# Optimization experiments

Measured on AMD Instinct MI355X. Metric: run time of the kernel, lower is better.

The kernel has to match this reference:

```python
import jax, jax.numpy as jnp
import numpy as np

B, C, W, H = 8, 64, 256, 256


def setup_inputs() -> dict:
    key = jax.random.key(0)
    ks = jax.random.split(key, 7)
    s = lambda n: 1.0 / np.sqrt(n)
    return {
        "x": jax.random.normal(ks[0], (B, C, W, H), dtype=jnp.float32),
        "Wc": jax.random.uniform(ks[1], (C, C), jnp.float32, -s(C), s(C)),
        "bc": jax.random.uniform(ks[2], (C,), jnp.float32, -s(C), s(C)),
        "Ww": jax.random.uniform(ks[3], (W, W), jnp.float32, -s(W), s(W)),
        "bw": jax.random.uniform(ks[4], (W,), jnp.float32, -s(W), s(W)),
        "Wh": jax.random.uniform(ks[5], (H, H), jnp.float32, -s(H), s(H)),
        "bh": jax.random.uniform(ks[6], (H,), jnp.float32, -s(H), s(H)),
    }


def reference(x, Wc, bc, Ww, bw, Wh, bh):
    # SE-style gates: global avg-pool over the two non-gated dims, 1x1 conv
    # (= dense on pooled vector), sigmoid. x is (B, C, W, H).
    c = jax.nn.sigmoid(jnp.einsum("oc,bc->bo", Wc, x.mean((2, 3))) + bc)  # (B, C)
    w = jax.nn.sigmoid(jnp.einsum("ow,bw->bo", Ww, x.mean((1, 3))) + bw)  # (B, W)
    h = jax.nn.sigmoid(jnp.einsum("oh,bh->bo", Wh, x.mean((1, 2))) + bh)  # (B, H)
    # Rank-1 tensor (triple outer product) per batch, broadcast-fused:
    return c[:, :, None, None] * w[:, None, :, None] * h[:, None, None, :]
```

## Files before the change

### kernel.cpp

```cpp
#include <hip/hip_runtime.h>


#define NB 8
#define NC 64
#define NW 256
#define NH 256

typedef float f4v __attribute__((ext_vector_type(4)));


__global__ __launch_bounds__(256) void pool_kernel(const float* __restrict__ x,
                                                   float* __restrict__ ws) {
    float* sum_c = ws;
    float* sum_w = ws + 512;
    float* sum_h = ws + 2560;

    int k    = blockIdx.x;
    int bc   = k >> 2;
    int q    = k & 3;
    int b    = bc >> 6;
    int tid  = threadIdx.x;
    int wv   = tid >> 6;
    int lane = tid & 63;

    const f4v* xr = (const f4v*)x + (size_t)bc * (NW * (NH / 4))
                    + (size_t)(q * 64 + wv * 16) * (NH / 4) + lane;

    __shared__ float rowsum[4][16];
    __shared__ float cols[4][NH];
    __shared__ float wpart[4];

    f4v v[16];
    #pragma unroll
    for (int r = 0; r < 16; ++r) v[r] = xr[(size_t)r * (NH / 4)];

    f4v col = {0.f, 0.f, 0.f, 0.f};
    float rs[16];
    #pragma unroll
    for (int r = 0; r < 16; ++r) {
        col += v[r];
        rs[r] = (v[r][0] + v[r][1]) + (v[r][2] + v[r][3]);
    }
    #pragma unroll
    for (int off = 32; off; off >>= 1) {
        #pragma unroll
        for (int r = 0; r < 16; ++r) rs[r] += __shfl_xor(rs[r], off);
    }
    #pragma unroll
    for (int r = 0; r < 16; ++r)
        if (lane == r) rowsum[wv][r] = rs[r];

    cols[wv][lane * 4 + 0] = col[0];
    cols[wv][lane * 4 + 1] = col[1];
    cols[wv][lane * 4 + 2] = col[2];
    cols[wv][lane * 4 + 3] = col[3];
    __syncthreads();

    float cv = cols[0][tid] + cols[1][tid] + cols[2][tid] + cols[3][tid];
    atomicAdd(&sum_h[b * NH + tid], cv);

    if (tid < 64)
        atomicAdd(&sum_w[b * NW + q * 64 + tid], rowsum[tid >> 4][tid & 15]);

    float t = cv;
    #pragma unroll
    for (int off = 32; off; off >>= 1) t += __shfl_xor(t, off);
    if (lane == 0) wpart[wv] = t;
    __syncthreads();
    if (tid == 0) atomicAdd(&sum_c[bc], wpart[0] + wpart[1] + wpart[2] + wpart[3]);
}

__global__ __launch_bounds__(256) void gates_kernel(const float* __restrict__ Wc, const float* __restrict__ bc_,
                                                    const float* __restrict__ Ww, const float* __restrict__ bw_,
                                                    const float* __restrict__ Wh, const float* __restrict__ bh_,
                                                    float* __restrict__ ws) {
    const float* sum_c = ws;
    const float* sum_w = ws + 512;
    const float* sum_h = ws + 2560;
    float* gate_c = ws + 4608;
    float* gate_w = ws + 5120;
    float* gate_h = ws + 7168;

    int j = blockIdx.x * 4 + (threadIdx.x >> 6);
    int lane = threadIdx.x & 63;

    float acc = 0.f, bias;
    float* dst;
    if (j < 512) {
        int b = j >> 6, o = j & 63;
        acc = Wc[o * 64 + lane] * sum_c[b * 64 + lane] * (1.f / 65536.f);
        bias = bc_[o];
        dst = &gate_c[j];
    } else if (j < 2560) {
        int j2 = j - 512;
        int b = j2 >> 8, o = j2 & 255;
        const float* wr = Ww + o * 256;
        const float* sr = sum_w + b * 256;
        #pragma unroll
        for (int m = 0; m < 4; ++m) acc += wr[lane + 64 * m] * sr[lane + 64 * m];
        acc *= (1.f / 16384.f);
        bias = bw_[o];
        dst = &gate_w[j2];
    } else {
        int j2 = j - 2560;
        int b = j2 >> 8, o = j2 & 255;
        const float* wr = Wh + o * 256;
        const float* sr = sum_h + b * 256;
        #pragma unroll
        for (int m = 0; m < 4; ++m) acc += wr[lane + 64 * m] * sr[lane + 64 * m];
        acc *= (1.f / 16384.f);
        bias = bh_[o];
        dst = &gate_h[j2];
    }
    #pragma unroll
    for (int off = 32; off; off >>= 1) acc += __shfl_xor(acc, off);
    if (lane == 0) *dst = 1.f / (1.f + expf(-(acc + bias)));
}

__global__ __launch_bounds__(256) void out_kernel(const float* __restrict__ ws,
                                                  float* __restrict__ out) {
    const float* gate_c = ws + 4608;
    const float* gate_w = ws + 5120;
    const float4* gate_h4 = (const float4*)(ws + 7168);

    const size_t N4 = (size_t)NB * NC * NW * (NH / 4);
    size_t stride = (size_t)gridDim.x * blockDim.x;
    for (size_t i = (size_t)blockIdx.x * blockDim.x + threadIdx.x; i < N4; i += stride) {
        int h4 = (int)(i & 63);
        size_t row = i >> 6;
        int w = (int)(row & 255);
        size_t bcr = row >> 8;
        int c = (int)(bcr & 63);
        int b = (int)(bcr >> 6);
        float g = gate_c[b * 64 + c] * gate_w[b * 256 + w];
        float4 gh = gate_h4[b * 64 + h4];
        f4v val = {g * gh.x, g * gh.y, g * gh.z, g * gh.w};
        __builtin_nontemporal_store(val, (f4v*)(out + 4 * i));
    }
}

extern "C" void kernel_launch(void* const* d_in, const int* in_sizes, int n_in,
                              void* d_out, int out_size, void* d_ws, size_t ws_size,
                              hipStream_t stream) {
    const float* x   = (const float*)d_in[0];
    const float* Wc  = (const float*)d_in[1];
    const float* bc_ = (const float*)d_in[2];
    const float* Ww  = (const float*)d_in[3];
    const float* bw_ = (const float*)d_in[4];
    const float* Wh  = (const float*)d_in[5];
    const float* bh_ = (const float*)d_in[6];
    float* ws = (float*)d_ws;

    hipMemsetAsync(ws, 0, 4608 * sizeof(float), stream);

    pool_kernel<<<2048, 256, 0, stream>>>(x, ws);
    gates_kernel<<<4608 / 4, 256, 0, stream>>>(Wc, bc_, Ww, bw_, Wh, bh_, ws);
    out_kernel<<<2048, 256, 0, stream>>>(ws, (float*)d_out);
}
```

Measured before the change: 62.80 us.

## Restructure pool kernel into 512-thread blocks covering half a plane with interleaved rows

The pooling kernel now uses 1024 blocks of 512 threads, each reducing half of a (b,c) plane (128 rows), instead of 2048 blocks of 256 threads over a quarter plane. Rows are interleaved across the 8 waves and loaded in two batches of 8 using nontemporal loads, which cuts register pressure and halves the number of atomics on sum_h. The trade is fewer blocks in flight, less memory-level parallelism per thread, and a more complex shared-memory reduction.

```diff
diff --git a/kernel.cpp b/kernel.cpp
--- a/kernel.cpp
+++ b/kernel.cpp
@@ -9,46 +9,49 @@
 typedef float f4v __attribute__((ext_vector_type(4)));
 
 
-__global__ __launch_bounds__(256) void pool_kernel(const float* __restrict__ x,
+__global__ __launch_bounds__(512) void pool_kernel(const float* __restrict__ x,
                                                    float* __restrict__ ws) {
     float* sum_c = ws;
     float* sum_w = ws + 512;
     float* sum_h = ws + 2560;
 
     int k    = blockIdx.x;
-    int bc   = k >> 2;
-    int q    = k & 3;
+    int bc   = k >> 1;
+    int half = k & 1;
     int b    = bc >> 6;
     int tid  = threadIdx.x;
     int wv   = tid >> 6;
     int lane = tid & 63;
+    int wbase = half * 128;
 
-    const f4v* xr = (const f4v*)x + (size_t)bc * (NW * (NH / 4))
-                    + (size_t)(q * 64 + wv * 16) * (NH / 4) + lane;
+    const f4v* xr = (const f4v*)x + (size_t)bc * (NW * (NH / 4));
 
-    __shared__ float rowsum[4][16];
-    __shared__ float cols[4][NH];
+    __shared__ float rowsum[8][16];
+    __shared__ float cols[8][NH];
     __shared__ float wpart[4];
 
-    f4v v[16];
-    #pragma unroll
-    for (int r = 0; r < 16; ++r) v[r] = xr[(size_t)r * (NH / 4)];
-
     f4v col = {0.f, 0.f, 0.f, 0.f};
-    float rs[16];
-    #pragma unroll
-    for (int r = 0; r < 16; ++r) {
-        col += v[r];
-        rs[r] = (v[r][0] + v[r][1]) + (v[r][2] + v[r][3]);
+    for (int jb = 0; jb < 16; jb += 8) {
+        f4v v[8];
+        #pragma unroll
+        for (int i = 0; i < 8; ++i)
+            v[i] = __builtin_nontemporal_load(
+                xr + (size_t)(wbase + wv + 8 * (jb + i)) * (NH / 4) + lane);
+        float rs[8];
+        #pragma unroll
+        for (int i = 0; i < 8; ++i) {
+            col += v[i];
+            rs[i] = (v[i][0] + v[i][1]) + (v[i][2] + v[i][3]);
+        }
+        #pragma unroll
+        for (int off = 32; off; off >>= 1) {
+            #pragma unroll
+            for (int i = 0; i < 8; ++i) rs[i] += __shfl_xor(rs[i], off);
+        }
+        #pragma unroll
+        for (int i = 0; i < 8; ++i)
+            if (lane == i) rowsum[wv][jb + i] = rs[i];
     }
-    #pragma unroll
-    for (int off = 32; off; off >>= 1) {
-        #pragma unroll
-        for (int r = 0; r < 16; ++r) rs[r] += __shfl_xor(rs[r], off);
-    }
-    #pragma unroll
-    for (int r = 0; r < 16; ++r)
-        if (lane == r) rowsum[wv][r] = rs[r];
 
     cols[wv][lane * 4 + 0] = col[0];
     cols[wv][lane * 4 + 1] = col[1];
@@ -56,18 +59,22 @@
     cols[wv][lane * 4 + 3] = col[3];
     __syncthreads();
 
-    float cv = cols[0][tid] + cols[1][tid] + cols[2][tid] + cols[3][tid];
-    atomicAdd(&sum_h[b * NH + tid], cv);
+    if (tid < 256) {
+        float cv = 0.f;
+        #pragma unroll
+        for (int w8 = 0; w8 < 8; ++w8) cv += cols[w8][tid];
+        atomicAdd(&sum_h[b * NH + tid], cv);
 
-    if (tid < 64)
-        atomicAdd(&sum_w[b * NW + q * 64 + tid], rowsum[tid >> 4][tid & 15]);
-
-    float t = cv;
-    #pragma unroll
-    for (int off = 32; off; off >>= 1) t += __shfl_xor(t, off);
-    if (lane == 0) wpart[wv] = t;
+        float t = cv;
+        #pragma unroll
+        for (int off = 32; off; off >>= 1) t += __shfl_xor(t, off);
+        if (lane == 0) wpart[wv] = t;
+    }
+    if (tid < 128)
+        atomicAdd(&sum_w[b * NW + wbase + tid], rowsum[tid & 7][tid >> 3]);
     __syncthreads();
-    if (tid == 0) atomicAdd(&sum_c[bc], wpart[0] + wpart[1] + wpart[2] + wpart[3]);
+    if (tid == 0)
+        atomicAdd(&sum_c[bc], (wpart[0] + wpart[1]) + (wpart[2] + wpart[3]));
 }
 
 __global__ __launch_bounds__(256) void gates_kernel(const float* __restrict__ Wc, const float* __restrict__ bc_,
@@ -153,7 +160,7 @@
 
     hipMemsetAsync(ws, 0, 4608 * sizeof(float), stream);
 
-    pool_kernel<<<2048, 256, 0, stream>>>(x, ws);
+    pool_kernel<<<1024, 512, 0, stream>>>(x, ws);
     gates_kernel<<<4608 / 4, 256, 0, stream>>>(Wc, bc_, Ww, bw_, Wh, bh_, ws);
     out_kernel<<<2048, 256, 0, stream>>>(ws, (float*)d_out);
 }
```

After: 57.49 us (median of 2 runs). 8.5% less time.
